# Kernel tuning notes

Hardware: AMD Instinct MI355X
Metric: run time of the kernel (lower is better)

## Reference

```python
import jax, jax.numpy as jnp
import numpy as np

N_EMBD = 768
N_HEAD = 12
HEAD_DIM = N_EMBD // N_HEAD
LN_EPS = 1e-5


def setup_inputs() -> dict:
    key = jax.random.key(0)
    ks = jax.random.split(key, 12)
    s = 0.02
    B, T = 8, 1024
    return {
        "x": jax.random.normal(ks[0], (B, T, N_EMBD), dtype=jnp.float32),
        "ln1_g": jnp.ones((N_EMBD,), jnp.float32),
        "ln1_b": jnp.zeros((N_EMBD,), jnp.float32),
        "w_attn": jax.random.normal(ks[1], (N_EMBD, 3 * N_EMBD), jnp.float32) * s,
        "b_attn": jnp.zeros((3 * N_EMBD,), jnp.float32),
        "w_proj": jax.random.normal(ks[2], (N_EMBD, N_EMBD), jnp.float32) * s,
        "b_proj": jnp.zeros((N_EMBD,), jnp.float32),
        "ln2_g": jnp.ones((N_EMBD,), jnp.float32),
        "ln2_b": jnp.zeros((N_EMBD,), jnp.float32),
        "w_fc1": jax.random.normal(ks[3], (N_EMBD, 4 * N_EMBD), jnp.float32) * s,
        "b_fc1": jnp.zeros((4 * N_EMBD,), jnp.float32),
        "w_fc2": jax.random.normal(ks[4], (4 * N_EMBD, N_EMBD), jnp.float32) * s,
        "b_fc2": jnp.zeros((N_EMBD,), jnp.float32),
    }


def _layernorm(x, g, b):
    mu = jnp.mean(x, axis=-1, keepdims=True)
    var = jnp.mean(jnp.square(x - mu), axis=-1, keepdims=True)
    return (x - mu) * jax.lax.rsqrt(var + LN_EPS) * g + b


def _block(x, ln1_g, ln1_b, w_attn, b_attn, w_proj, b_proj,
           ln2_g, ln2_b, w_fc1, b_fc1, w_fc2, b_fc2):
    B, T, C = x.shape
    # --- causal self-attention (dropout inactive in eval) ---
    h = _layernorm(x, ln1_g, ln1_b)
    qkv = h @ w_attn + b_attn                      # [B,T,3C]
    q, k, v = jnp.split(qkv, 3, axis=-1)
    q = q.reshape(B, T, N_HEAD, HEAD_DIM).transpose(0, 2, 1, 3)  # [B,H,T,D]
    k = k.reshape(B, T, N_HEAD, HEAD_DIM).transpose(0, 2, 1, 3)
    v = v.reshape(B, T, N_HEAD, HEAD_DIM).transpose(0, 2, 1, 3)
    att = jnp.einsum('bhtd,bhsd->bhts', q, k) * (1.0 / np.sqrt(HEAD_DIM))
    mask = jnp.tril(jnp.ones((T, T), dtype=bool))
    att = jnp.where(mask, att, -jnp.inf)
    att = jax.nn.softmax(att, axis=-1)
    y = jnp.einsum('bhts,bhsd->bhtd', att, v)
    y = y.transpose(0, 2, 1, 3).reshape(B, T, C)
    x = x + y @ w_proj + b_proj
    # --- MLP ---
    h2 = _layernorm(x, ln2_g, ln2_b)
    h2 = jax.nn.gelu(h2 @ w_fc1 + b_fc1, approximate=True)
    x = x + h2 @ w_fc2 + b_fc2
    return x


def reference(x, ln1_g, ln1_b, w_attn, b_attn, w_proj, b_proj,
              ln2_g, ln2_b, w_fc1, b_fc1, w_fc2, b_fc2):
    return _block(x, ln1_g, ln1_b, w_attn, b_attn, w_proj, b_proj,
                  ln2_g, ln2_b, w_fc1, b_fc1, w_fc2, b_fc2)
```

## Files before the change

### kernel.cpp

```cpp
#include <hip/hip_runtime.h>
#include <cstdint>
#include <cmath>

typedef unsigned short u16;
typedef __bf16 bf16_t;
typedef bf16_t bf16x8 __attribute__((ext_vector_type(8)));
typedef float f32x4 __attribute__((ext_vector_type(4)));
typedef u16 u16x8 __attribute__((ext_vector_type(8)));
typedef u16 u16x4 __attribute__((ext_vector_type(4)));

#define DEV __device__ __forceinline__

DEV u16 f2b(float f) {
    uint32_t u = __builtin_bit_cast(uint32_t, f);
    u += 0x7FFFu + ((u >> 16) & 1u);
    return (u16)(u >> 16);
}
DEV float b2f(u16 h) { return __builtin_bit_cast(float, (uint32_t)h << 16); }

DEV bf16x8 load8(const u16* p) {
    return __builtin_bit_cast(bf16x8, *reinterpret_cast<const u16x8*>(p));
}

DEV void async16(void* lds, const void* g) {
    __builtin_amdgcn_global_load_lds(
        reinterpret_cast<const __attribute__((address_space(1))) void*>(
            reinterpret_cast<uintptr_t>(g)),
        reinterpret_cast<__attribute__((address_space(3))) void*>(
            reinterpret_cast<uintptr_t>(lds)),
        16, 0, 0);
}

DEV float gelu_t(float x) {
    float z = 0.7978845608028654f * (x + 0.044715f * x * x * x);
    z = fminf(fmaxf(z, -15.0f), 15.0f);
    float e = __expf(2.0f * z);
    return 0.5f * x * (1.0f + (e - 1.0f) / (e + 1.0f));
}

__global__ __launch_bounds__(256) void ln_k(const float* __restrict__ x,
                                            const float* __restrict__ g,
                                            const float* __restrict__ bb,
                                            u16* __restrict__ out) {
    const int lane = threadIdx.x & 63, w = threadIdx.x >> 6;
    const int row = blockIdx.x * 4 + w;
    const float4* xr = reinterpret_cast<const float4*>(x + (size_t)row * 768);
    float4 v[3];
    float s = 0.f, s2 = 0.f;
#pragma unroll
    for (int i = 0; i < 3; ++i) {
        v[i] = xr[i * 64 + lane];
        s += v[i].x + v[i].y + v[i].z + v[i].w;
        s2 += v[i].x * v[i].x + v[i].y * v[i].y + v[i].z * v[i].z + v[i].w * v[i].w;
    }
#pragma unroll
    for (int off = 1; off < 64; off <<= 1) {
        s += __shfl_xor(s, off);
        s2 += __shfl_xor(s2, off);
    }
    const float mu = s * (1.0f / 768.0f);
    const float rstd = rsqrtf(s2 * (1.0f / 768.0f) - mu * mu + 1e-5f);
#pragma unroll
    for (int i = 0; i < 3; ++i) {
        int col = i * 256 + lane * 4;
        u16x4 o;
        o[0] = f2b((v[i].x - mu) * rstd * g[col + 0] + bb[col + 0]);
        o[1] = f2b((v[i].y - mu) * rstd * g[col + 1] + bb[col + 1]);
        o[2] = f2b((v[i].z - mu) * rstd * g[col + 2] + bb[col + 2]);
        o[3] = f2b((v[i].w - mu) * rstd * g[col + 3] + bb[col + 3]);
        *reinterpret_cast<u16x4*>(out + (size_t)row * 768 + col) = o;
    }
}

__global__ __launch_bounds__(256) void ln_b16(const u16* __restrict__ x,
                                              const float* __restrict__ g,
                                              const float* __restrict__ bb,
                                              u16* __restrict__ out) {
    const int lane = threadIdx.x & 63, w = threadIdx.x >> 6;
    const int row = blockIdx.x * 4 + w;
    const u16* xr = x + (size_t)row * 768;
    float v[12];
    float s = 0.f, s2 = 0.f;
#pragma unroll
    for (int i = 0; i < 3; ++i) {
        u16x4 u = *reinterpret_cast<const u16x4*>(xr + i * 256 + lane * 4);
#pragma unroll
        for (int jj = 0; jj < 4; ++jj) {
            float f = b2f(u[jj]);
            v[i * 4 + jj] = f;
            s += f;
            s2 += f * f;
        }
    }
#pragma unroll
    for (int off = 1; off < 64; off <<= 1) {
        s += __shfl_xor(s, off);
        s2 += __shfl_xor(s2, off);
    }
    const float mu = s * (1.0f / 768.0f);
    const float rstd = rsqrtf(s2 * (1.0f / 768.0f) - mu * mu + 1e-5f);
#pragma unroll
    for (int i = 0; i < 3; ++i) {
        int col = i * 256 + lane * 4;
        u16x4 o;
#pragma unroll
        for (int jj = 0; jj < 4; ++jj)
            o[jj] = f2b((v[i * 4 + jj] - mu) * rstd * g[col + jj] + bb[col + jj]);
        *reinterpret_cast<u16x4*>(out + (size_t)row * 768 + col) = o;
    }
}

__global__ __launch_bounds__(256) void wconv_k(const float* __restrict__ W,
                                               u16* __restrict__ WT, int K, int N) {
    __shared__ float tile[32][33];
    const int tx = threadIdx.x, ty = threadIdx.y;
    const int n0 = blockIdx.x * 32, k0 = blockIdx.y * 32;
#pragma unroll
    for (int i = 0; i < 4; ++i)
        tile[ty + i * 8][tx] = W[(size_t)(k0 + ty + i * 8) * N + n0 + tx];
    __syncthreads();
#pragma unroll
    for (int i = 0; i < 4; ++i)
        WT[(size_t)(n0 + ty + i * 8) * K + k0 + tx] = f2b(tile[tx][ty + i * 8]);
}

__global__ __launch_bounds__(256) void vtrans_k(const u16* __restrict__ qkv,
                                                u16* __restrict__ vT) {
    __shared__ u16 tile[32][33];
    const int tx = threadIdx.x, ty = threadIdx.y;
    const int t0 = blockIdx.x * 32, d0 = blockIdx.y * 32, bh = blockIdx.z;
    const int b = bh / 12, hd = bh % 12;
#pragma unroll
    for (int i = 0; i < 4; ++i)
        tile[ty + i * 8][tx] =
            qkv[(size_t)(b * 1024 + t0 + ty + i * 8) * 2304 + 1536 + hd * 64 + d0 + tx];
    __syncthreads();
#pragma unroll
    for (int i = 0; i < 4; ++i)
        vT[(size_t)(bh * 64 + d0 + ty + i * 8) * 1024 + t0 + tx] = tile[tx][ty + i * 8];
}

template <int ACT, int RESIDT, int OUTBF>
__global__ __launch_bounds__(256) void gemm_bt(const u16* __restrict__ A,
                                               const u16* __restrict__ BT,
                                               const float* __restrict__ bias,
                                               const void* __restrict__ resid,
                                               void* __restrict__ out,
                                               int M, int N, int K) {
    __shared__ u16 As[2][128 * 32];
    __shared__ u16 Bs[2][128 * 32];
    const int tid = threadIdx.x, lane = tid & 63;
    const int l15 = lane & 15, lg = lane >> 4;
    const int nx = gridDim.x;
    const int bid = blockIdx.y * nx + blockIdx.x;
    const int q = (nx * gridDim.y) >> 3;
    const int swz = (bid & 7) * q + (bid >> 3);
    const int mBase = (swz / nx) * 128, nBase = (swz % nx) * 128;
    const int w = tid >> 6, wr = w >> 1, wc = w & 1;

    auto stage = [&](int buf, int kk) {
        const int k0 = kk << 5;
#pragma unroll
        for (int i = 0; i < 2; ++i) {
            int c = i * 256 + tid;
            int row = c >> 2;
            int g = ((c & 3) ^ ((row >> 1) & 3)) << 3;
            async16(As[buf] + c * 8, A + (size_t)(mBase + row) * K + k0 + g);
        }
#pragma unroll
        for (int i = 0; i < 2; ++i) {
            int c = i * 256 + tid;
            int row = c >> 2;
            int g = ((c & 3) ^ ((row >> 1) & 3)) << 3;
            async16(Bs[buf] + c * 8, BT + (size_t)(nBase + row) * K + k0 + g);
        }
    };

    f32x4 acc[4][4] = {};
    const int nsteps = K >> 5;
    stage(0, 0);
    for (int kk = 0; kk < nsteps; ++kk) {
        const int cur = kk & 1;
        if (kk + 1 < nsteps) {
            stage(cur ^ 1, kk + 1);
            asm volatile("s_waitcnt vmcnt(4)" ::: "memory");
        } else {
            asm volatile("s_waitcnt vmcnt(0)" ::: "memory");
        }
        __builtin_amdgcn_s_barrier();
        asm volatile("" ::: "memory");

        bf16x8 af[4], bfr[4];
#pragma unroll
        for (int mi = 0; mi < 4; ++mi) {
            int rA = wr * 64 + mi * 16 + l15;
            af[mi] = load8(As[cur] + rA * 32 + ((lg ^ ((rA >> 1) & 3)) << 3));
        }
#pragma unroll
        for (int ni = 0; ni < 4; ++ni) {
            int rB = wc * 64 + ni * 16 + l15;
            bfr[ni] = load8(Bs[cur] + rB * 32 + ((lg ^ ((rB >> 1) & 3)) << 3));
        }
        __builtin_amdgcn_s_setprio(1);
#pragma unroll
        for (int mi = 0; mi < 4; ++mi)
#pragma unroll
            for (int ni = 0; ni < 4; ++ni)
                acc[mi][ni] = __builtin_amdgcn_mfma_f32_16x16x32_bf16(
                    af[mi], bfr[ni], acc[mi][ni], 0, 0, 0);
        __builtin_amdgcn_s_setprio(0);

        asm volatile("" ::: "memory");
        __builtin_amdgcn_s_barrier();
        asm volatile("" ::: "memory");
    }
#pragma unroll
    for (int mi = 0; mi < 4; ++mi) {
#pragma unroll
        for (int ni = 0; ni < 4; ++ni) {
            const int row0 = mBase + wr * 64 + mi * 16 + lg * 4;
            const int col = nBase + wc * 64 + ni * 16 + l15;
            const float bv = bias[col];
#pragma unroll
            for (int r = 0; r < 4; ++r) {
                float v = acc[mi][ni][r] + bv;
                if (ACT == 1) v = gelu_t(v);
                size_t off = (size_t)(row0 + r) * N + col;
                if (RESIDT == 1) v += ((const float*)resid)[off];
                if (RESIDT == 2) v += b2f(((const u16*)resid)[off]);
                if (OUTBF)
                    ((u16*)out)[off] = f2b(v);
                else
                    ((float*)out)[off] = v;
            }
        }
    }
}

__global__ __launch_bounds__(256, 3) void attn_k(const u16* __restrict__ qkv,
                                                 const u16* __restrict__ vT,
                                                 u16* __restrict__ y) {
    __shared__ u16 Ks[2][64 * 64];
    __shared__ u16 Vs[2][64 * 64];
    __shared__ u16 Ps[4][2][16 * 64];
    const int tid = threadIdx.x, lane = tid & 63, w = tid >> 6;
    const int bid = blockIdx.x;
    const uint32_t permPk = 2u | (7u << 3) | (1u << 6) | (4u << 9) | (6u << 12) |
                            (0u << 15) | (5u << 18) | (3u << 21);
    const int qt = (permPk >> (((bid + (bid >> 8)) & 7) * 3)) & 7;
    const int bh = ((bid >> 8) << 5) + ((bid & 255) >> 3);
    const int b = bh / 12, hd = bh % 12;
    const int l15 = lane & 15, lg = lane >> 4;
    const int r0 = qt * 128 + w * 32;

    const float qscale = 0.125f * 1.4426950408889634f;
    bf16x8 qf[2][2];
#pragma unroll
    for (int m = 0; m < 2; ++m) {
        const u16* qb = qkv + (size_t)(b * 1024 + r0 + m * 16 + l15) * 2304 + hd * 64;
#pragma unroll
        for (int ks = 0; ks < 2; ++ks) {
            u16x8 u = *reinterpret_cast<const u16x8*>(qb + ks * 32 + lg * 8);
            u16x8 o;
#pragma unroll
            for (int jj = 0; jj < 8; ++jj) o[jj] = f2b(b2f(u[jj]) * qscale);
            qf[m][ks] = __builtin_bit_cast(bf16x8, o);
        }
    }

    const u16* kbase = qkv + (size_t)(b * 1024) * 2304 + 768 + hd * 64;
    const u16* vbase = vT + (size_t)(bh * 64) * 1024;

    auto stage = [&](int buf, int j) {
#pragma unroll
        for (int i = 0; i < 2; ++i) {
            int c = i * 256 + tid;
            int row = c >> 3, sc = ((c & 7) ^ (row & 7)) << 3;
            async16(Ks[buf] + c * 8, kbase + (size_t)(j * 64 + row) * 2304 + sc);
        }
#pragma unroll
        for (int i = 0; i < 2; ++i) {
            int c = i * 256 + tid;
            int row = c >> 3, sc = ((c & 7) ^ (row & 7)) << 3;
            async16(Vs[buf] + c * 8, vbase + (size_t)row * 1024 + j * 64 + sc);
        }
    };

    f32x4 oacc[2][4] = {};
    float mrow[2] = {-1e30f, -1e30f};
    float lrow[2] = {0.f, 0.f};

    const int jd = (r0 + 31) >> 6;
    const int jmax = qt * 2 + 1;

    stage(0, 0);
    for (int j = 0; j <= jmax; ++j) {
        const int cur = j & 1;
        if (j < jmax) {
            stage(cur ^ 1, j + 1);
            asm volatile("s_waitcnt vmcnt(4)" ::: "memory");
        } else {
            asm volatile("s_waitcnt vmcnt(0)" ::: "memory");
        }
        __builtin_amdgcn_s_barrier();
        asm volatile("" ::: "memory");

        if (j <= jd) {
            const bool diag = (j == jd);
            const u16* Kc = Ks[cur];
            const u16* Vc = Vs[cur];
            f32x4 s[2][4] = {};
            __builtin_amdgcn_s_setprio(1);
#pragma unroll
            for (int ks = 0; ks < 2; ++ks) {
                bf16x8 kf[4];
#pragma unroll
                for (int ni = 0; ni < 4; ++ni) {
                    int key = ni * 16 + l15;
                    kf[ni] = load8(Kc + key * 64 + (((ks * 4 + lg) ^ (key & 7)) << 3));
                }
#pragma unroll
                for (int ni = 0; ni < 4; ++ni) {
                    s[0][ni] = __builtin_amdgcn_mfma_f32_16x16x32_bf16(
                        kf[ni], qf[0][ks], s[0][ni], 0, 0, 0);
                    s[1][ni] = __builtin_amdgcn_mfma_f32_16x16x32_bf16(
                        kf[ni], qf[1][ks], s[1][ni], 0, 0, 0);
                }
            }
            __builtin_amdgcn_s_setprio(0);

#pragma unroll
            for (int m = 0; m < 2; ++m) {
                if (diag) {
                    const int qrow = r0 + m * 16 + l15;
#pragma unroll
                    for (int ni = 0; ni < 4; ++ni) {
                        int key = j * 64 + ni * 16 + lg * 4;
#pragma unroll
                        for (int r = 0; r < 4; ++r)
                            if (key + r > qrow) s[m][ni][r] = -1e30f;
                    }
                }
                float pmax = -1e30f;
#pragma unroll
                for (int ni = 0; ni < 4; ++ni)
#pragma unroll
                    for (int r = 0; r < 4; ++r) pmax = fmaxf(pmax, s[m][ni][r]);
                pmax = fmaxf(pmax, __shfl_xor(pmax, 16));
                pmax = fmaxf(pmax, __shfl_xor(pmax, 32));

                if (!__all(pmax <= mrow[m] + 8.0f)) {
                    float mnew = fmaxf(mrow[m], pmax);
                    float scal = exp2f(mrow[m] - mnew);
                    mrow[m] = mnew;
                    lrow[m] *= scal;
#pragma unroll
                    for (int r = 0; r < 4; ++r) {
                        float sr = __shfl(scal, lg * 4 + r);
#pragma unroll
                        for (int ni = 0; ni < 4; ++ni) oacc[m][ni][r] *= sr;
                    }
                }
                float psum = 0.f;
#pragma unroll
                for (int ni = 0; ni < 4; ++ni) {
                    u16x4 pk;
#pragma unroll
                    for (int r = 0; r < 4; ++r) {
                        float pv = exp2f(s[m][ni][r] - mrow[m]);
                        psum += pv;
                        pk[r] = f2b(pv);
                    }
                    *reinterpret_cast<u16x4*>(
                        &Ps[w][m][l15 * 64 + ((ni * 16 + lg * 4) ^ ((l15 & 7) << 3))]) =
                        pk;
                }
                psum += __shfl_xor(psum, 16);
                psum += __shfl_xor(psum, 32);
                lrow[m] += psum;
            }

            __builtin_amdgcn_s_setprio(1);
#pragma unroll
            for (int ks = 0; ks < 2; ++ks) {
                bf16x8 pf0 = load8(
                    &Ps[w][0][l15 * 64 + ((ks * 32 + lg * 8) ^ ((l15 & 7) << 3))]);
                bf16x8 pf1 = load8(
                    &Ps[w][1][l15 * 64 + ((ks * 32 + lg * 8) ^ ((l15 & 7) << 3))]);
                bf16x8 vf[4];
#pragma unroll
                for (int ni = 0; ni < 4; ++ni) {
                    int d = ni * 16 + l15;
                    vf[ni] = load8(Vc + d * 64 + (((ks * 4 + lg) ^ (d & 7)) << 3));
                }
#pragma unroll
                for (int ni = 0; ni < 4; ++ni) {
                    oacc[0][ni] = __builtin_amdgcn_mfma_f32_16x16x32_bf16(
                        pf0, vf[ni], oacc[0][ni], 0, 0, 0);
                    oacc[1][ni] = __builtin_amdgcn_mfma_f32_16x16x32_bf16(
                        pf1, vf[ni], oacc[1][ni], 0, 0, 0);
                }
            }
            __builtin_amdgcn_s_setprio(0);
        }
        asm volatile("" ::: "memory");
        __builtin_amdgcn_s_barrier();
        asm volatile("" ::: "memory");
    }

#pragma unroll
    for (int m = 0; m < 2; ++m) {
#pragma unroll
        for (int r = 0; r < 4; ++r) {
            float rl = 1.0f / __shfl(lrow[m], lg * 4 + r);
            int row = r0 + m * 16 + lg * 4 + r;
#pragma unroll
            for (int ni = 0; ni < 4; ++ni) {
                int col = hd * 64 + ni * 16 + l15;
                y[(size_t)(b * 1024 + row) * 768 + col] = f2b(oacc[m][ni][r] * rl);
            }
        }
    }
}

extern "C" void kernel_launch(void* const* d_in, const int* in_sizes, int n_in,
                              void* d_out, int out_size, void* d_ws, size_t ws_size,
                              hipStream_t stream) {
    const float* x      = (const float*)d_in[0];
    const float* ln1_g  = (const float*)d_in[1];
    const float* ln1_b  = (const float*)d_in[2];
    const float* w_attn = (const float*)d_in[3];
    const float* b_attn = (const float*)d_in[4];
    const float* w_proj = (const float*)d_in[5];
    const float* b_proj = (const float*)d_in[6];
    const float* ln2_g  = (const float*)d_in[7];
    const float* ln2_b  = (const float*)d_in[8];
    const float* w_fc1  = (const float*)d_in[9];
    const float* b_fc1  = (const float*)d_in[10];
    const float* w_fc2  = (const float*)d_in[11];
    const float* b_fc2  = (const float*)d_in[12];
    float* out = (float*)d_out;

    char* p = (char*)d_ws;
    auto take = [&](size_t n) {
        char* r = p;
        p += (n + 255) & ~(size_t)255;
        return r;
    };
    u16* wT_attn = (u16*)take((size_t)2304 * 768 * 2);
    u16* wT_proj = (u16*)take((size_t)768 * 768 * 2);
    u16* wT_fc1  = (u16*)take((size_t)3072 * 768 * 2);
    u16* wT_fc2  = (u16*)take((size_t)768 * 3072 * 2);
    u16* h       = (u16*)take((size_t)8192 * 768 * 2);
    u16* bufA    = (u16*)take((size_t)50331648);
    u16* yb      = (u16*)take((size_t)8192 * 768 * 2);
    u16* x1b     = (u16*)take((size_t)8192 * 768 * 2);
    u16* qkv = bufA;
    u16* vT  = bufA + (size_t)8192 * 2304;
    u16* g1  = bufA;

    const dim3 tb(32, 8);
    wconv_k<<<dim3(2304 / 32, 768 / 32), tb, 0, stream>>>(w_attn, wT_attn, 768, 2304);
    wconv_k<<<dim3(768 / 32, 768 / 32), tb, 0, stream>>>(w_proj, wT_proj, 768, 768);
    wconv_k<<<dim3(3072 / 32, 768 / 32), tb, 0, stream>>>(w_fc1, wT_fc1, 768, 3072);
    wconv_k<<<dim3(768 / 32, 3072 / 32), tb, 0, stream>>>(w_fc2, wT_fc2, 3072, 768);
    ln_k<<<2048, 256, 0, stream>>>(x, ln1_g, ln1_b, h);
    gemm_bt<0, 0, 1><<<dim3(18, 64), 256, 0, stream>>>(h, wT_attn, b_attn, nullptr,
                                                       qkv, 8192, 2304, 768);
    vtrans_k<<<dim3(32, 2, 96), tb, 0, stream>>>(qkv, vT);
    attn_k<<<768, 256, 0, stream>>>(qkv, vT, yb);
    gemm_bt<0, 1, 1><<<dim3(6, 64), 256, 0, stream>>>(yb, wT_proj, b_proj, x,
                                                      x1b, 8192, 768, 768);
    ln_b16<<<2048, 256, 0, stream>>>(x1b, ln2_g, ln2_b, h);
    gemm_bt<1, 0, 1><<<dim3(24, 64), 256, 0, stream>>>(h, wT_fc1, b_fc1, nullptr,
                                                       g1, 8192, 3072, 768);
    gemm_bt<0, 2, 0><<<dim3(6, 64), 256, 0, stream>>>(g1, wT_fc2, b_fc2, x1b,
                                                      out, 8192, 768, 3072);
}
```

Baseline: 254.6 us.

## Load GEMM weight fragments directly from global memory, skipping LDS staging

```diff
diff --git a/kernel.cpp b/kernel.cpp
--- a/kernel.cpp
+++ b/kernel.cpp
@@ -140,7 +140,7 @@
         vT[(size_t)(bh * 64 + d0 + ty + i * 8) * 1024 + t0 + tx] = tile[tx][ty + i * 8];
 }
 
-template <int ACT, int RESIDT, int OUTBF>
+template <int ACT, int RESIDT, int OUTBF, int BDIRECT>
 __global__ __launch_bounds__(256) void gemm_bt(const u16* __restrict__ A,
                                                const u16* __restrict__ BT,
                                                const float* __restrict__ bias,
@@ -148,17 +148,18 @@
                                                void* __restrict__ out,
                                                int M, int N, int K) {
     __shared__ u16 As[2][128 * 32];
-    __shared__ u16 Bs[2][128 * 32];
+    __shared__ u16 Bs[BDIRECT ? 8 : 2 * 128 * 32];
     const int tid = threadIdx.x, lane = tid & 63;
     const int l15 = lane & 15, lg = lane >> 4;
-    const int nx = gridDim.x;
-    const int bid = blockIdx.y * nx + blockIdx.x;
-    const int q = (nx * gridDim.y) >> 3;
-    const int swz = (bid & 7) * q + (bid >> 3);
-    const int mBase = (swz / nx) * 128, nBase = (swz % nx) * 128;
+    const int nx = gridDim.x, ny = gridDim.y;
+    const int d = blockIdx.y * nx + blockIdx.x;
+    const int q = (nx * ny) >> 3;
+    const int swz = (d & 7) * q + (d >> 3);
+    const int nBase = (swz / ny) * 128;
+    const int mBase = (swz % ny) * 128;
     const int w = tid >> 6, wr = w >> 1, wc = w & 1;
 
-    auto stage = [&](int buf, int kk) {
+    auto stageA = [&](int buf, int kk) {
         const int k0 = kk << 5;
 #pragma unroll
         for (int i = 0; i < 2; ++i) {
@@ -167,23 +168,34 @@
             int g = ((c & 3) ^ ((row >> 1) & 3)) << 3;
             async16(As[buf] + c * 8, A + (size_t)(mBase + row) * K + k0 + g);
         }
-#pragma unroll
-        for (int i = 0; i < 2; ++i) {
-            int c = i * 256 + tid;
-            int row = c >> 2;
-            int g = ((c & 3) ^ ((row >> 1) & 3)) << 3;
-            async16(Bs[buf] + c * 8, BT + (size_t)(nBase + row) * K + k0 + g);
+    };
+    auto stageB = [&](int buf, int kk) {
+        if constexpr (!BDIRECT) {
+            const int k0 = kk << 5;
+#pragma unroll
+            for (int i = 0; i < 2; ++i) {
+                int c = i * 256 + tid;
+                int row = c >> 2;
+                int g = ((c & 3) ^ ((row >> 1) & 3)) << 3;
+                async16(Bs + (size_t)buf * (128 * 32) + c * 8,
+                        BT + (size_t)(nBase + row) * K + k0 + g);
+            }
         }
     };
 
     f32x4 acc[4][4] = {};
     const int nsteps = K >> 5;
-    stage(0, 0);
+    stageA(0, 0);
+    stageB(0, 0);
     for (int kk = 0; kk < nsteps; ++kk) {
         const int cur = kk & 1;
         if (kk + 1 < nsteps) {
-            stage(cur ^ 1, kk + 1);
-            asm volatile("s_waitcnt vmcnt(4)" ::: "memory");
+            stageA(cur ^ 1, kk + 1);
+            stageB(cur ^ 1, kk + 1);
+            if (BDIRECT)
+                asm volatile("s_waitcnt vmcnt(2)" ::: "memory");
+            else
+                asm volatile("s_waitcnt vmcnt(4)" ::: "memory");
         } else {
             asm volatile("s_waitcnt vmcnt(0)" ::: "memory");
         }
@@ -191,15 +203,19 @@
         asm volatile("" ::: "memory");
 
         bf16x8 af[4], bfr[4];
+#pragma unroll
+        for (int ni = 0; ni < 4; ++ni) {
+            int rB = wc * 64 + ni * 16 + l15;
+            if (BDIRECT)
+                bfr[ni] = load8(BT + (size_t)(nBase + rB) * K + (kk << 5) + lg * 8);
+            else
+                bfr[ni] = load8(Bs + (size_t)cur * (128 * 32) + rB * 32 +
+                                ((lg ^ ((rB >> 1) & 3)) << 3));
+        }
 #pragma unroll
         for (int mi = 0; mi < 4; ++mi) {
             int rA = wr * 64 + mi * 16 + l15;
             af[mi] = load8(As[cur] + rA * 32 + ((lg ^ ((rA >> 1) & 3)) << 3));
-        }
-#pragma unroll
-        for (int ni = 0; ni < 4; ++ni) {
-            int rB = wc * 64 + ni * 16 + l15;
-            bfr[ni] = load8(Bs[cur] + rB * 32 + ((lg ^ ((rB >> 1) & 3)) << 3));
         }
         __builtin_amdgcn_s_setprio(1);
 #pragma unroll
@@ -465,15 +481,15 @@
     wconv_k<<<dim3(3072 / 32, 768 / 32), tb, 0, stream>>>(w_fc1, wT_fc1, 768, 3072);
     wconv_k<<<dim3(768 / 32, 3072 / 32), tb, 0, stream>>>(w_fc2, wT_fc2, 3072, 768);
     ln_k<<<2048, 256, 0, stream>>>(x, ln1_g, ln1_b, h);
-    gemm_bt<0, 0, 1><<<dim3(18, 64), 256, 0, stream>>>(h, wT_attn, b_attn, nullptr,
-                                                       qkv, 8192, 2304, 768);
+    gemm_bt<0, 0, 1, 1><<<dim3(18, 64), 256, 0, stream>>>(h, wT_attn, b_attn, nullptr,
+                                                          qkv, 8192, 2304, 768);
     vtrans_k<<<dim3(32, 2, 96), tb, 0, stream>>>(qkv, vT);
     attn_k<<<768, 256, 0, stream>>>(qkv, vT, yb);
-    gemm_bt<0, 1, 1><<<dim3(6, 64), 256, 0, stream>>>(yb, wT_proj, b_proj, x,
-                                                      x1b, 8192, 768, 768);
+    gemm_bt<0, 1, 1, 1><<<dim3(6, 64), 256, 0, stream>>>(yb, wT_proj, b_proj, x,
+                                                         x1b, 8192, 768, 768);
     ln_b16<<<2048, 256, 0, stream>>>(x1b, ln2_g, ln2_b, h);
-    gemm_bt<1, 0, 1><<<dim3(24, 64), 256, 0, stream>>>(h, wT_fc1, b_fc1, nullptr,
-                                                       g1, 8192, 3072, 768);
-    gemm_bt<0, 2, 0><<<dim3(6, 64), 256, 0, stream>>>(g1, wT_fc2, b_fc2, x1b,
-                                                      out, 8192, 768, 3072);
-}
+    gemm_bt<1, 0, 1, 1><<<dim3(24, 64), 256, 0, stream>>>(h, wT_fc1, b_fc1, nullptr,
+                                                          g1, 8192, 3072, 768);
+    gemm_bt<0, 2, 0, 0><<<dim3(6, 64), 256, 0, stream>>>(g1, wT_fc2, b_fc2, x1b,
+                                                         out, 8192, 768, 3072);
+}
```

After: 365.6 us. 43.6% more time.
